# Kernel tuning notes

Hardware: AMD Instinct MI355X
Metric: run time of the kernel (lower is better)

## Reference

```python
import jax, jax.numpy as jnp
import numpy as np
from jax import lax

VOCAB, E, H = 32000, 256, 512
B, T = 64, 1024


def setup_inputs() -> dict:
    key = jax.random.key(0)
    ks = jax.random.split(key, 5)
    tokens = jax.random.randint(ks[0], (B, T), 0, VOCAB, dtype=jnp.int64 if jax.config.jax_enable_x64 else jnp.int32).astype(jnp.int32)
    emb_table = jax.random.normal(ks[1], (VOCAB, E), dtype=jnp.float32) * 0.02
    W_x = jax.random.normal(ks[2], (E, 4 * H), dtype=jnp.float32) * 0.02
    W_h = jax.random.normal(ks[3], (H, 4 * H), dtype=jnp.float32) * 0.02
    b = jnp.zeros((4 * H,), dtype=jnp.float32)
    h0 = jnp.zeros((B, H), dtype=jnp.float32)
    c0 = jnp.zeros((B, H), dtype=jnp.float32)
    return {"tokens": tokens, "h0": h0, "c0": c0, "emb_table": emb_table,
            "W_x": W_x, "W_h": W_h, "b": b}


def reference(tokens, h0, c0, emb_table, W_x, W_h, b):
    # Embedding lookup with mask_zero=True semantics: token 0 is padding.
    x = emb_table[tokens]                      # [B, T, E]
    mask = tokens != 0                         # [B, T]
    # Precompute input projections for all timesteps (same math, one GEMM).
    xz = jnp.einsum('bte,ef->btf', x, W_x) + b  # [B, T, 4H]

    def step(carry, inp):
        h, c = carry
        xzt, mt = inp                          # [B,4H], [B]
        z = xzt + h @ W_h                      # [B, 4H]
        i, f, g, o = jnp.split(z, 4, axis=-1)  # Keras gate order: i, f, c, o
        i = jax.nn.sigmoid(i)
        f = jax.nn.sigmoid(f)
        g = jnp.tanh(g)
        o = jax.nn.sigmoid(o)
        c_new = f * c + i * g
        h_new = o * jnp.tanh(c_new)
        m = mt[:, None]
        # Masked steps carry previous state/output (Keras masking behavior).
        h = jnp.where(m, h_new, h)
        c = jnp.where(m, c_new, c)
        return (h, c), h

    (h_T, c_T), outs = lax.scan(step, (h0, c0),
                                (xz.transpose(1, 0, 2), mask.T))
    return outs.transpose(1, 0, 2), h_T, c_T  # [B,T,H], [B,H], [B,H]
```

## Files before the change

kernel.cpp:

```cpp
#include <hip/hip_runtime.h>
#include <hip/hip_bf16.h>

#define B_ 64
#define T_ 1024
#define E_ 256
#define H_ 512
#define ZN_ 2048
#define NSLICE 64
#define KT_ 24

typedef short bf16x8 __attribute__((ext_vector_type(8)));
typedef float f32x4 __attribute__((ext_vector_type(4)));
typedef int i32x4 __attribute__((ext_vector_type(4)));

union frag_u { i32x4 i; bf16x8 h; };

__device__ __forceinline__ short f2bf(float f) {
  union { float f; unsigned u; } v; v.f = f;
  unsigned r = v.u + 0x7fffu + ((v.u >> 16) & 1u);
  return (short)(r >> 16);
}
__device__ __forceinline__ float sigmoidf_(float x) {
  return 1.f / (1.f + __expf(-x));
}
__device__ __forceinline__ float tanhf_(float x) {
  x = fminf(10.f, fmaxf(-10.f, x));
  float e = __expf(2.f * x);
  return (e - 1.f) / (e + 1.f);
}

__device__ __forceinline__ i32x4 ld_sys(const void* p) {
  i32x4 r;
  asm volatile("global_load_dwordx4 %0, %1, off sc0 sc1" : "=v"(r) : "v"(p) : "memory");
  return r;
}
__device__ __forceinline__ void st_sys(void* p, i32x4 v) {
  asm volatile("global_store_dwordx4 %0, %1, off sc0 sc1" :: "v"(p), "v"(v) : "memory");
}
__device__ __forceinline__ int ld_sys_poll(const int* p) {
  int r;
  asm volatile("global_load_dword %0, %1, off sc0 sc1\n\ts_waitcnt vmcnt(0)"
               : "=v"(r) : "v"(p) : "memory");
  return r;
}
__device__ __forceinline__ void st_sys_i32(int* p, int v) {
  asm volatile("global_store_dword %0, %1, off sc0 sc1" :: "v"(p), "v"(v) : "memory");
}


__global__ void k_emb_cvt(const float* __restrict__ emb, short* __restrict__ dst, int n8) {
  int i = blockIdx.x * blockDim.x + threadIdx.x;
  if (i >= n8) return;
  const float4* s = (const float4*)emb;
  float4 a = s[2 * i], b = s[2 * i + 1];
  bf16x8 o;
  o[0] = f2bf(a.x); o[1] = f2bf(a.y); o[2] = f2bf(a.z); o[3] = f2bf(a.w);
  o[4] = f2bf(b.x); o[5] = f2bf(b.y); o[6] = f2bf(b.z); o[7] = f2bf(b.w);
  ((bf16x8*)dst)[i] = o;
}

__global__ void k_wfrag(const float* __restrict__ Wx, const float* __restrict__ Wh,
                        short* __restrict__ wf) {
  int tid = blockIdx.x * blockDim.x + threadIdx.x;
  if (tid >= NSLICE * 2 * KT_ * 64) return;
  int lane = tid & 63;
  int kt = (tid >> 6) % KT_;
  int nt = (tid >> 6) / KT_ % 2;
  int s = tid / (64 * KT_ * 2);
  int c16 = lane & 15, ksub = lane >> 4;
  int g = c16 & 3, hc = c16 >> 2;
  int zcol = g * H_ + s * 8 + nt * 4 + hc;
  int k0 = kt * 32 + ksub * 8;
  bf16x8 o;
#pragma unroll
  for (int i = 0; i < 8; ++i) {
    int k = k0 + i;
    float v = (k < E_) ? Wx[(size_t)k * ZN_ + zcol] : Wh[(size_t)(k - E_) * ZN_ + zcol];
    o[i] = f2bf(v);
  }
  ((bf16x8*)wf)[tid] = o;
}

__global__ void k_tok(const int* __restrict__ tok, int* __restrict__ tokT,
                      unsigned long long* __restrict__ mask) {
  int t = blockIdx.x * blockDim.x + threadIdx.x;
  if (t >= T_) return;
  unsigned long long m = 0ull;
  for (int b = 0; b < B_; ++b) {
    int tk = tok[b * T_ + t];
    tokT[t * B_ + b] = tk;
    if (tk != 0) m |= (1ull << b);
  }
  mask[t] = m;
}

__global__ void k_init(const float* __restrict__ h0, short* __restrict__ hbuf0,
                       int* __restrict__ flags) {
  int i = blockIdx.x * blockDim.x + threadIdx.x;
  if (i < 1024) flags[i] = 0;
  if (i >= B_ * H_) return;
  hbuf0[i] = f2bf(h0[i]);
}


__global__ __launch_bounds__(512) void k_lstm(
    const int* __restrict__ tokT, const short* __restrict__ emb,
    const short* __restrict__ wf, const float* __restrict__ bias,
    const unsigned long long* __restrict__ maskv,
    short* __restrict__ hb0, short* __restrict__ hb1,
    const float* __restrict__ h0, const float* __restrict__ c0,
    float* __restrict__ out, int* __restrict__ flags)
{
  __shared__ __align__(16) short hlocBF[B_][8];

  int s = blockIdx.x;
  int w = threadIdx.x >> 6, l = threadIdx.x & 63;
  int mtile = w & 3, ntile = w >> 2;
  int c16 = l & 15, ksub = l >> 4;
  int g = c16 & 3, hc = c16 >> 2;
  int arow = mtile * 16 + c16;
  int lcol = ntile * 4 + hc;
  int col = s * 8 + lcol;
  const int* myflag = flags + l * 16;

  bf16x8 wreg[KT_];
  {
    const bf16x8* bp = (const bf16x8*)wf + ((size_t)(s * 2 + ntile) * KT_) * 64 + l;
#pragma unroll
    for (int kt = 0; kt < KT_; ++kt) wreg[kt] = bp[kt * 64];
  }
  float zb = bias[g * H_ + col];

  float cst[4], hst[4];
#pragma unroll
  for (int r = 0; r < 4; ++r) {
    int row = mtile * 16 + ksub * 4 + r;
    cst[r] = c0[row * H_ + col];
    hst[r] = h0[row * H_ + col];
  }

  auto compute_x = [&](int t) -> f32x4 {
    int tk = tokT[t * B_ + arow];
    const bf16x8* ax = (const bf16x8*)emb + (size_t)tk * 32 + ksub;
    f32x4 a0 = {0.f, 0.f, 0.f, 0.f}, a1 = {0.f, 0.f, 0.f, 0.f};
#pragma unroll
    for (int kt = 0; kt < 8; kt += 2) {
      a0 = __builtin_amdgcn_mfma_f32_16x16x32_bf16(ax[kt * 4], wreg[kt], a0, 0, 0, 0);
      a1 = __builtin_amdgcn_mfma_f32_16x16x32_bf16(ax[(kt + 1) * 4], wreg[kt + 1], a1, 0, 0, 0);
    }
    return a0 + a1;
  };

  f32x4 accx = compute_x(0);

  for (int t = 0; t < T_; ++t) {
    const short* hr = (t & 1) ? hb1 : hb0;
    short* hw       = (t & 1) ? hb0 : hb1;

    if (t > 0) {
      for (;;) {
        int v = ld_sys_poll(myflag);
        if (__all(v >= t)) break;
        __builtin_amdgcn_s_sleep(1);
      }
    }

    const short* hbase = hr + arow * H_ + ksub * 8;
    frag_u hf[16];
#pragma unroll
    for (int kt = 0; kt < 16; ++kt)
      hf[kt].i = ld_sys(hbase + kt * 32);
    asm volatile("s_waitcnt vmcnt(0)" ::: "memory");
    __builtin_amdgcn_sched_barrier(0);

    f32x4 acc = accx;
    f32x4 b0 = {0.f, 0.f, 0.f, 0.f};
#pragma unroll
    for (int kt = 0; kt < 16; kt += 2) {
      acc = __builtin_amdgcn_mfma_f32_16x16x32_bf16(hf[kt].h, wreg[8 + kt], acc, 0, 0, 0);
      b0  = __builtin_amdgcn_mfma_f32_16x16x32_bf16(hf[kt + 1].h, wreg[9 + kt], b0, 0, 0, 0);
    }
    acc += b0;

    float act[4];
#pragma unroll
    for (int r = 0; r < 4; ++r) {
      float z = acc[r] + zb;
      act[r] = (g == 2) ? tanhf_(z) : sigmoidf_(z);
    }

    unsigned long long mk = maskv[t];
    int base = l & ~3;
#pragma unroll
    for (int r = 0; r < 4; ++r) {
      float fs = __shfl(act[r], base + 1);
      float gt = __shfl(act[r], base + 2);
      float os = __shfl(act[r], base + 3);
      if (g == 0) {
        int row = mtile * 16 + ksub * 4 + r;
        bool mm = (mk >> row) & 1ull;
        float cn = fs * cst[r] + act[r] * gt;
        float hn = os * tanhf_(cn);
        if (mm) { cst[r] = cn; hst[r] = hn; }
        hlocBF[row][lcol] = f2bf(hst[r]);
      }
    }

    __syncthreads();

    if (w == 0) {
      frag_u v; v.h = *(const bf16x8*)&hlocBF[l][0];
      st_sys(hw + l * H_ + s * 8, v.i);
      asm volatile("s_waitcnt vmcnt(0)" ::: "memory");
      if (l == 0) st_sys_i32((int*)(flags + s * 16), t + 1);
    }

    if (g == 0) {
#pragma unroll
      for (int r = 0; r < 4; ++r) {
        int row = mtile * 16 + ksub * 4 + r;
        __builtin_nontemporal_store(hst[r], out + ((size_t)row * T_ + t) * H_ + col);
      }
    }
    if (t == T_ - 1 && g == 0) {
#pragma unroll
      for (int r = 0; r < 4; ++r) {
        int row = mtile * 16 + ksub * 4 + r;
        out[(size_t)B_ * T_ * H_ + row * H_ + col] = hst[r];
        out[(size_t)B_ * T_ * H_ + B_ * H_ + row * H_ + col] = cst[r];
      }
    }

    if (t + 1 < T_) accx = compute_x(t + 1);
  }
}


extern "C" void kernel_launch(void* const* d_in, const int* in_sizes, int n_in,
                              void* d_out, int out_size, void* d_ws, size_t ws_size,
                              hipStream_t stream) {
  (void)in_sizes; (void)n_in; (void)out_size; (void)ws_size;
  const int* tokens = (const int*)d_in[0];
  const float* h0 = (const float*)d_in[1];
  const float* c0 = (const float*)d_in[2];
  const float* emb = (const float*)d_in[3];
  const float* Wx = (const float*)d_in[4];
  const float* Wh = (const float*)d_in[5];
  const float* bias = (const float*)d_in[6];
  float* out = (float*)d_out;
  char* ws = (char*)d_ws;

  short* emb_bf = (short*)(ws);
  short* wf     = (short*)(ws + 16384000);
  unsigned long long* mask = (unsigned long long*)(ws + 19529728);
  int* tokT     = (int*)(ws + 19537920);
  short* hb0    = (short*)(ws + 19800064);
  short* hb1    = (short*)(ws + 19800064 + 65536);
  int* flags    = (int*)(ws + 19931136);

  k_emb_cvt<<<(1024000 + 255) / 256, 256, 0, stream>>>(emb, emb_bf, 1024000);
  k_wfrag<<<(NSLICE * 2 * KT_ * 64 + 255) / 256, 256, 0, stream>>>(Wx, Wh, wf);
  k_tok<<<(T_ + 255) / 256, 256, 0, stream>>>(tokens, tokT, mask);
  k_init<<<(B_ * H_ + 255) / 256, 256, 0, stream>>>(h0, hb0, flags);

  k_lstm<<<NSLICE, 512, 0, stream>>>(tokT, emb_bf, wf, bias, mask,
                                     hb0, hb1, h0, c0, out, flags);
}
```

Before: 7.511 ms.

## Specialize warps: 4 compute waves, dedicated poller and output-store waves

The 512-thread LSTM block is restructured so only four waves do the recurrent MFMA work, each covering both N-tiles and sharing one set of h fragments. Wave 4 polls the cross-block flags and publishes h, and waves 5-6 write the output sequence from a new fp32 shared staging buffer. The input-projection weights move from registers to LDS. This halves the global h loads per step and takes the output stores off the critical path, but doubles the MFMA chain per compute wave and adds extra barriers per step.

Result: faster. 6.291 ms (-16.2%).

```diff
diff --git a/kernel.cpp b/kernel.cpp
--- a/kernel.cpp
+++ b/kernel.cpp
@@ -7,22 +7,26 @@
 #define H_ 512
 #define ZN_ 2048
 #define NSLICE 64
-#define KT_ 24
+#define KTX 8
+#define KTH 16
+#define KT_ (KTX + KTH)
 
 typedef short bf16x8 __attribute__((ext_vector_type(8)));
 typedef float f32x4 __attribute__((ext_vector_type(4)));
 typedef int i32x4 __attribute__((ext_vector_type(4)));
 
 union frag_u { i32x4 i; bf16x8 h; };
+
+#define RAW_BAR() __builtin_amdgcn_s_barrier()
+#define LGKM0() asm volatile("s_waitcnt lgkmcnt(0)" ::: "memory")
+#define VM0() asm volatile("s_waitcnt vmcnt(0)" ::: "memory")
 
 __device__ __forceinline__ short f2bf(float f) {
   union { float f; unsigned u; } v; v.f = f;
   unsigned r = v.u + 0x7fffu + ((v.u >> 16) & 1u);
   return (short)(r >> 16);
 }
-__device__ __forceinline__ float sigmoidf_(float x) {
-  return 1.f / (1.f + __expf(-x));
-}
+__device__ __forceinline__ float sigmoidf_(float x) { return 1.f / (1.f + __expf(-x)); }
 __device__ __forceinline__ float tanhf_(float x) {
   x = fminf(10.f, fmaxf(-10.f, x));
   float e = __expf(2.f * x);
@@ -103,7 +107,7 @@
 }
 
 
-__global__ __launch_bounds__(512) void k_lstm(
+__global__ __launch_bounds__(512, 2) void k_lstm(
     const int* __restrict__ tokT, const short* __restrict__ emb,
     const short* __restrict__ wf, const float* __restrict__ bias,
     const unsigned long long* __restrict__ maskv,
@@ -111,127 +115,148 @@
     const float* __restrict__ h0, const float* __restrict__ c0,
     float* __restrict__ out, int* __restrict__ flags)
 {
+  __shared__ __align__(16) short x_wf[2 * KTX * 64 * 8];
+  __shared__ __align__(16) float hlocF[B_][8];
   __shared__ __align__(16) short hlocBF[B_][8];
 
   int s = blockIdx.x;
   int w = threadIdx.x >> 6, l = threadIdx.x & 63;
-  int mtile = w & 3, ntile = w >> 2;
   int c16 = l & 15, ksub = l >> 4;
   int g = c16 & 3, hc = c16 >> 2;
-  int arow = mtile * 16 + c16;
-  int lcol = ntile * 4 + hc;
-  int col = s * 8 + lcol;
-  const int* myflag = flags + l * 16;
-
-  bf16x8 wreg[KT_];
-  {
-    const bf16x8* bp = (const bf16x8*)wf + ((size_t)(s * 2 + ntile) * KT_) * 64 + l;
-#pragma unroll
-    for (int kt = 0; kt < KT_; ++kt) wreg[kt] = bp[kt * 64];
-  }
-  float zb = bias[g * H_ + col];
-
-  float cst[4], hst[4];
-#pragma unroll
-  for (int r = 0; r < 4; ++r) {
-    int row = mtile * 16 + ksub * 4 + r;
-    cst[r] = c0[row * H_ + col];
-    hst[r] = h0[row * H_ + col];
-  }
-
-  auto compute_x = [&](int t) -> f32x4 {
+  int base = l & ~3;
+  int arow = w * 16 + c16;
+
+  for (int idx = threadIdx.x; idx < 2 * KTX * 64; idx += 512) {
+    int lane = idx & 63;
+    int ktn = idx >> 6;
+    int nt = ktn / KTX, kt = ktn % KTX;
+    ((bf16x8*)x_wf)[idx] = ((const bf16x8*)wf)[(((size_t)(s * 2 + nt)) * KT_ + kt) * 64 + lane];
+  }
+
+  bf16x8 wreg0[KTH], wreg1[KTH];
+  float zb0 = 0.f, zb1 = 0.f;
+  float cst[2][4], hst[2][4];
+  if (w < 4) {
+    const bf16x8* b0 = (const bf16x8*)wf + (((size_t)(s * 2 + 0)) * KT_ + KTX) * 64 + l;
+    const bf16x8* b1 = (const bf16x8*)wf + (((size_t)(s * 2 + 1)) * KT_ + KTX) * 64 + l;
+#pragma unroll
+    for (int kt = 0; kt < KTH; ++kt) { wreg0[kt] = b0[kt * 64]; wreg1[kt] = b1[kt * 64]; }
+    zb0 = bias[g * H_ + s * 8 + 0 + hc];
+    zb1 = bias[g * H_ + s * 8 + 4 + hc];
+#pragma unroll
+    for (int j = 0; j < 2; ++j) {
+      int col = s * 8 + j * 4 + hc;
+#pragma unroll
+      for (int r = 0; r < 4; ++r) {
+        int row = w * 16 + ksub * 4 + r;
+        cst[j][r] = c0[row * H_ + col];
+        hst[j][r] = h0[row * H_ + col];
+      }
+    }
+  }
+  LGKM0();
+  RAW_BAR();
+
+  f32x4 accx0 = {0.f, 0.f, 0.f, 0.f}, accx1 = {0.f, 0.f, 0.f, 0.f};
+  auto compute_x = [&](int t) {
     int tk = tokT[t * B_ + arow];
     const bf16x8* ax = (const bf16x8*)emb + (size_t)tk * 32 + ksub;
     f32x4 a0 = {0.f, 0.f, 0.f, 0.f}, a1 = {0.f, 0.f, 0.f, 0.f};
 #pragma unroll
-    for (int kt = 0; kt < 8; kt += 2) {
-      a0 = __builtin_amdgcn_mfma_f32_16x16x32_bf16(ax[kt * 4], wreg[kt], a0, 0, 0, 0);
-      a1 = __builtin_amdgcn_mfma_f32_16x16x32_bf16(ax[(kt + 1) * 4], wreg[kt + 1], a1, 0, 0, 0);
-    }
-    return a0 + a1;
+    for (int kt = 0; kt < KTX; ++kt) {
+      bf16x8 a = ax[kt * 4];
+      a0 = __builtin_amdgcn_mfma_f32_16x16x32_bf16(a, ((const bf16x8*)x_wf)[(0 * KTX + kt) * 64 + l], a0, 0, 0, 0);
+      a1 = __builtin_amdgcn_mfma_f32_16x16x32_bf16(a, ((const bf16x8*)x_wf)[(1 * KTX + kt) * 64 + l], a1, 0, 0, 0);
+    }
+    accx0 = a0; accx1 = a1;
   };
 
-  f32x4 accx = compute_x(0);
+  if (w < 4) compute_x(0);
 
   for (int t = 0; t < T_; ++t) {
     const short* hr = (t & 1) ? hb1 : hb0;
     short* hw       = (t & 1) ? hb0 : hb1;
 
-    if (t > 0) {
+    if (w == 4 && t > 0) {
       for (;;) {
-        int v = ld_sys_poll(myflag);
+        int v = ld_sys_poll(flags + l * 16);
         if (__all(v >= t)) break;
         __builtin_amdgcn_s_sleep(1);
       }
     }
-
-    const short* hbase = hr + arow * H_ + ksub * 8;
-    frag_u hf[16];
-#pragma unroll
-    for (int kt = 0; kt < 16; ++kt)
-      hf[kt].i = ld_sys(hbase + kt * 32);
-    asm volatile("s_waitcnt vmcnt(0)" ::: "memory");
-    __builtin_amdgcn_sched_barrier(0);
-
-    f32x4 acc = accx;
-    f32x4 b0 = {0.f, 0.f, 0.f, 0.f};
-#pragma unroll
-    for (int kt = 0; kt < 16; kt += 2) {
-      acc = __builtin_amdgcn_mfma_f32_16x16x32_bf16(hf[kt].h, wreg[8 + kt], acc, 0, 0, 0);
-      b0  = __builtin_amdgcn_mfma_f32_16x16x32_bf16(hf[kt + 1].h, wreg[9 + kt], b0, 0, 0, 0);
-    }
-    acc += b0;
-
-    float act[4];
-#pragma unroll
-    for (int r = 0; r < 4; ++r) {
-      float z = acc[r] + zb;
-      act[r] = (g == 2) ? tanhf_(z) : sigmoidf_(z);
-    }
-
-    unsigned long long mk = maskv[t];
-    int base = l & ~3;
-#pragma unroll
-    for (int r = 0; r < 4; ++r) {
-      float fs = __shfl(act[r], base + 1);
-      float gt = __shfl(act[r], base + 2);
-      float os = __shfl(act[r], base + 3);
-      if (g == 0) {
-        int row = mtile * 16 + ksub * 4 + r;
-        bool mm = (mk >> row) & 1ull;
-        float cn = fs * cst[r] + act[r] * gt;
-        float hn = os * tanhf_(cn);
-        if (mm) { cst[r] = cn; hst[r] = hn; }
-        hlocBF[row][lcol] = f2bf(hst[r]);
-      }
-    }
-
-    __syncthreads();
-
-    if (w == 0) {
+    RAW_BAR();
+
+    if (w < 4) {
+      const short* hbase = hr + arow * H_ + ksub * 8;
+      frag_u hf[KTH];
+#pragma unroll
+      for (int kt = 0; kt < KTH; ++kt) hf[kt].i = ld_sys(hbase + kt * 32);
+      VM0();
+      __builtin_amdgcn_sched_barrier(0);
+
+      f32x4 ac0 = accx0, ac1 = accx1;
+#pragma unroll
+      for (int kt = 0; kt < KTH; ++kt) {
+        ac0 = __builtin_amdgcn_mfma_f32_16x16x32_bf16(hf[kt].h, wreg0[kt], ac0, 0, 0, 0);
+        ac1 = __builtin_amdgcn_mfma_f32_16x16x32_bf16(hf[kt].h, wreg1[kt], ac1, 0, 0, 0);
+      }
+
+      unsigned long long mk = maskv[t];
+#pragma unroll
+      for (int j = 0; j < 2; ++j) {
+        float zb = (j == 0) ? zb0 : zb1;
+        int lc = j * 4 + hc;
+        float act[4];
+#pragma unroll
+        for (int r = 0; r < 4; ++r) {
+          float z = ((j == 0) ? ac0[r] : ac1[r]) + zb;
+          act[r] = (g == 2) ? tanhf_(z) : sigmoidf_(z);
+        }
+#pragma unroll
+        for (int r = 0; r < 4; ++r) {
+          float fs = __shfl(act[r], base + 1);
+          float gt = __shfl(act[r], base + 2);
+          float os = __shfl(act[r], base + 3);
+          if (g == 0) {
+            int row = w * 16 + ksub * 4 + r;
+            bool mm = (mk >> row) & 1ull;
+            float cn = fs * cst[j][r] + act[r] * gt;
+            float hn = os * tanhf_(cn);
+            if (mm) { cst[j][r] = cn; hst[j][r] = hn; }
+            hlocF[row][lc] = hst[j][r];
+            hlocBF[row][lc] = f2bf(hst[j][r]);
+          }
+        }
+      }
+    }
+    LGKM0();
+    RAW_BAR();
+
+    if (w == 4) {
       frag_u v; v.h = *(const bf16x8*)&hlocBF[l][0];
       st_sys(hw + l * H_ + s * 8, v.i);
-      asm volatile("s_waitcnt vmcnt(0)" ::: "memory");
-      if (l == 0) st_sys_i32((int*)(flags + s * 16), t + 1);
-    }
-
-    if (g == 0) {
-#pragma unroll
-      for (int r = 0; r < 4; ++r) {
-        int row = mtile * 16 + ksub * 4 + r;
-        __builtin_nontemporal_store(hst[r], out + ((size_t)row * T_ + t) * H_ + col);
-      }
-    }
-    if (t == T_ - 1 && g == 0) {
-#pragma unroll
-      for (int r = 0; r < 4; ++r) {
-        int row = mtile * 16 + ksub * 4 + r;
-        out[(size_t)B_ * T_ * H_ + row * H_ + col] = hst[r];
-        out[(size_t)B_ * T_ * H_ + B_ * H_ + row * H_ + col] = cst[r];
-      }
-    }
-
-    if (t + 1 < T_) accx = compute_x(t + 1);
+      VM0();
+      if (l == 0) st_sys_i32(flags + s * 16, t + 1);
+    } else if (w == 5 || w == 6) {
+      int p = (w - 5) * 64 + l;
+      int row = p >> 1, half = p & 1;
+      f32x4 v = *(const f32x4*)&hlocF[row][half * 4];
+      __builtin_nontemporal_store(v, (f32x4*)(out + ((size_t)row * T_ + t) * H_ + s * 8 + half * 4));
+    } else if (w < 4) {
+      if (t == T_ - 1 && g == 0) {
+#pragma unroll
+        for (int j = 0; j < 2; ++j) {
+          int col = s * 8 + j * 4 + hc;
+#pragma unroll
+          for (int r = 0; r < 4; ++r) {
+            int row = w * 16 + ksub * 4 + r;
+            out[(size_t)B_ * T_ * H_ + row * H_ + col] = hst[j][r];
+            out[(size_t)B_ * T_ * H_ + B_ * H_ + row * H_ + col] = cst[j][r];
+          }
+        }
+      }
+      if (t + 1 < T_) compute_x(t + 1);
+    }
   }
 }
 
@@ -255,7 +280,7 @@
   unsigned long long* mask = (unsigned long long*)(ws + 19529728);
   int* tokT     = (int*)(ws + 19537920);
   short* hb0    = (short*)(ws + 19800064);
-  short* hb1    = (short*)(ws + 19800064 + 65536);
+  short* hb1    = (short*)(ws + 19865600);
   int* flags    = (int*)(ws + 19931136);
 
   k_emb_cvt<<<(1024000 + 255) / 256, 256, 0, stream>>>(emb, emb_bf, 1024000);
```
